# Optimization experiments

Hardware: AMD Instinct MI355X
Metric: run time of the kernel (lower is better)

The kernel has to match this reference:

```python
import jax, jax.numpy as jnp
import numpy as np

B, S, D_MODEL, D_K, D_V = 8, 2048, 1024, 1024, 1024


def setup_inputs() -> dict:
    key = jax.random.key(0)
    k1, k2, k3, k4 = jax.random.split(key, 4)
    x = jax.random.normal(k1, (B, S, D_MODEL), dtype=jnp.float32)
    # Store projection weights as [d_model, d_out] so projection is x @ W
    # (equivalent to torch Linear(d_model, d_out, bias=False) with W^T).
    scale = 1.0 / np.sqrt(D_MODEL)
    Wq = jax.random.normal(k2, (D_MODEL, D_K), dtype=jnp.float32) * scale
    Wk = jax.random.normal(k3, (D_MODEL, D_K), dtype=jnp.float32) * scale
    Wv = jax.random.normal(k4, (D_MODEL, D_V), dtype=jnp.float32) * scale
    return {"x": x, "Wq": Wq, "Wk": Wk, "Wv": Wv}


def reference(x, Wq, Wk, Wv):
    # Single-head causal self-attention, faithful to the original:
    # NOTE: the original scales by sqrt(x.shape[-1]) == sqrt(d_model),
    # not sqrt(d_k of the projection).
    Q = jnp.einsum('bsd,dk->bsk', x, Wq)
    K = jnp.einsum('bsd,dk->bsk', x, Wk)
    V = jnp.einsum('bsd,dv->bsv', x, Wv)
    inv_scale = 1.0 / jnp.sqrt(jnp.asarray(x.shape[-1], x.dtype))
    A = jnp.einsum('bqk,bsk->bqs', Q, K) * inv_scale  # [B, S, S]
    S_len = A.shape[-1]
    causal = jnp.tril(jnp.ones((S_len, S_len), dtype=bool))  # [S, S]
    A = jnp.where(causal, A, -jnp.inf)
    P = jax.nn.softmax(A, axis=-1)
    return jnp.einsum('bqs,bsv->bqv', P, V)
```

## Files before the change

### kernel.cpp

```cpp
#include <hip/hip_runtime.h>
#include <hip/hip_bf16.h>
#include <stdint.h>


typedef __bf16 bf16_t;
typedef __bf16 bf16x4 __attribute__((ext_vector_type(4)));
typedef __bf16 bf16x8 __attribute__((ext_vector_type(8)));
typedef float  floatx4 __attribute__((ext_vector_type(4)));

#define NB 8
#define SS 2048
#define DD 1024
#define INV_SCALE 0.03125f

__device__ __forceinline__ void async_ld16(const void* g, void* l) {
  __builtin_amdgcn_global_load_lds(
      (const __attribute__((address_space(1))) void*)g,
      (__attribute__((address_space(3))) void*)l, 16, 0, 0);
}

#define BARRIER() do { asm volatile("" ::: "memory"); \
  __builtin_amdgcn_s_barrier(); asm volatile("" ::: "memory"); } while (0)

__device__ __forceinline__ void mm256_core(
    const bf16_t* __restrict__ Ab, const bf16_t* __restrict__ Bb,
    int lda, int ldb, int nt,
    bf16_t* sA0, bf16_t* sA1, bf16_t* sA2, bf16_t* sA3,
    bf16_t* sB0, bf16_t* sB1, bf16_t* sB2, bf16_t* sB3,
    floatx4 acc[8][4]) {
  const int t    = threadIdx.x;
  const int lane = t & 63;
  const int wid  = t >> 6;
  const int wm   = wid >> 2;
  const int wn   = wid & 3;
  const int fm   = lane & 15;
  const int q    = lane >> 4;
  const int co   = (q ^ ((fm >> 1) & 3)) * 8;

  size_t goA[2], goB[2]; int lo[2];
#pragma unroll
  for (int k = 0; k < 2; ++k) {
    const int u   = k * 512 + t;
    const int row = u >> 2;
    const int cg  = (u & 3) ^ ((row >> 1) & 3);
    goA[k] = (size_t)row * lda + cg * 8;
    goB[k] = (size_t)row * ldb + cg * 8;
    lo[k]  = u * 8;
  }

  auto stage = [&](bf16_t* la, bf16_t* lb, int tile) {
    const size_t ko = (size_t)tile * 32;
    async_ld16(Ab + ko + goA[0], la + lo[0]);
    async_ld16(Ab + ko + goA[1], la + lo[1]);
    async_ld16(Bb + ko + goB[0], lb + lo[0]);
    async_ld16(Bb + ko + goB[1], lb + lo[1]);
  };

  const int paOff = (wm * 128 + fm) * 32;
  const int pbOff = (wn * 64 + fm) * 32;

  auto body = [&] __attribute__((always_inline)) (
      const bf16_t* AP, const bf16_t* BP, bf16_t* AN, bf16_t* BN, int T) {
    if (T + 3 < nt) {
      stage(AN, BN, T + 3);
      asm volatile("s_waitcnt vmcnt(12)" ::: "memory");
    } else if (T + 2 < nt) {
      asm volatile("s_waitcnt vmcnt(8)" ::: "memory");
    } else if (T + 1 < nt) {
      asm volatile("s_waitcnt vmcnt(4)" ::: "memory");
    } else {
      asm volatile("s_waitcnt vmcnt(0)" ::: "memory");
    }
    __builtin_amdgcn_s_barrier();
    asm volatile("" ::: "memory");

    const bf16_t* pa = AP + paOff;
    const bf16_t* pb = BP + pbOff;
    bf16x8 a0[4], a1[4], bv[4];
#pragma unroll
    for (int i = 0; i < 4; ++i) a0[i] = *(const bf16x8*)(pa + i * 512 + co);
#pragma unroll
    for (int j = 0; j < 4; ++j) bv[j] = *(const bf16x8*)(pb + j * 512 + co);
    __builtin_amdgcn_sched_barrier(0);
#pragma unroll
    for (int i = 0; i < 4; ++i) a1[i] = *(const bf16x8*)(pa + (4 + i) * 512 + co);

    asm volatile("s_waitcnt lgkmcnt(4)" ::: "memory");
    __builtin_amdgcn_sched_barrier(0);
    __builtin_amdgcn_s_setprio(1);
#pragma unroll
    for (int i = 0; i < 4; ++i)
#pragma unroll
      for (int j = 0; j < 4; ++j)
        acc[i][j] = __builtin_amdgcn_mfma_f32_16x16x32_bf16(bv[j], a0[i], acc[i][j], 0, 0, 0);
    __builtin_amdgcn_s_setprio(0);

    asm volatile("s_waitcnt lgkmcnt(0)" ::: "memory");
    __builtin_amdgcn_sched_barrier(0);
    __builtin_amdgcn_s_setprio(1);
#pragma unroll
    for (int i = 0; i < 4; ++i)
#pragma unroll
      for (int j = 0; j < 4; ++j)
        acc[4 + i][j] = __builtin_amdgcn_mfma_f32_16x16x32_bf16(bv[j], a1[i], acc[4 + i][j], 0, 0, 0);
    __builtin_amdgcn_s_setprio(0);
    asm volatile("" ::: "memory");
    __builtin_amdgcn_s_barrier();
  };

  stage(sA0, sB0, 0);
  stage(sA1, sB1, 1);
  stage(sA2, sB2, 2);

  for (int tb = 0; tb < nt; tb += 4) {
    body(sA0, sB0, sA3, sB3, tb + 0);
    body(sA1, sB1, sA0, sB0, tb + 1);
    body(sA2, sB2, sA1, sB1, tb + 2);
    body(sA3, sB3, sA2, sB2, tb + 3);
  }
}

__device__ __forceinline__ void zero_acc8(floatx4 acc[8][4]) {
#pragma unroll
  for (int i = 0; i < 8; ++i)
#pragma unroll
    for (int j = 0; j < 4; ++j)
      acc[i][j] = floatx4{0.f, 0.f, 0.f, 0.f};
}

__device__ __forceinline__ void store_c256_bf16(bf16_t* __restrict__ Cb, int ldc,
                                                floatx4 acc[8][4]) {
  const int lane = threadIdx.x & 63;
  const int wid  = threadIdx.x >> 6;
  const int wm = wid >> 2, wn = wid & 3;
  const int m0 = wm * 128 + (lane & 15);
  const int n0 = wn * 64 + (lane >> 4) * 4;
#pragma unroll
  for (int i = 0; i < 8; ++i)
#pragma unroll
    for (int j = 0; j < 4; ++j) {
      floatx4 a = acc[i][j];
      bf16x4 o = {(bf16_t)a[0], (bf16_t)a[1], (bf16_t)a[2], (bf16_t)a[3]};
      *(bf16x4*)(Cb + (size_t)(m0 + i * 16) * ldc + n0 + j * 16) = o;
    }
}

#define MM256_LDS_DECL                                                      \
  __shared__ __attribute__((aligned(16))) bf16_t sA0[8192], sA1[8192],      \
      sA2[8192], sA3[8192];                                                 \
  __shared__ __attribute__((aligned(16))) bf16_t sB0[8192], sB1[8192],      \
      sB2[8192], sB3[8192];

__device__ __forceinline__ void mm_core2(
    const bf16_t* __restrict__ Ab, const bf16_t* __restrict__ Bb,
    int lda, int ldb, int nt,
    bf16_t* sA0, bf16_t* sB0, bf16_t* sA1, bf16_t* sB1,
    floatx4 acc[4][4]) {
  const int t    = threadIdx.x;
  const int lane = t & 63;
  const int wm   = (t >> 6) >> 1;
  const int wn   = (t >> 6) & 1;
  const int fm   = lane & 15;
  const int q    = lane >> 4;
  const int xo   = fm & 7;

  size_t goA[4], goB[4]; int lo[4];
#pragma unroll
  for (int k = 0; k < 4; ++k) {
    const int u   = k * 256 + t;
    const int row = u >> 3;
    const int cc  = (u & 7) ^ (row & 7);
    goA[k] = (size_t)row * lda + cc * 8;
    goB[k] = (size_t)row * ldb + cc * 8;
    lo[k]  = u * 8;
  }

  auto stage = [&](bf16_t* la, bf16_t* lb, int tile) {
    const size_t ko = (size_t)tile * 64;
#pragma unroll
    for (int k = 0; k < 4; ++k) async_ld16(Ab + ko + goA[k], la + lo[k]);
#pragma unroll
    for (int k = 0; k < 4; ++k) async_ld16(Bb + ko + goB[k], lb + lo[k]);
  };

  const int paOff = (wm * 64 + fm) * 64;
  const int pbOff = (wn * 64 + fm) * 64;

  auto body = [&] __attribute__((always_inline)) (
      const bf16_t* CA, const bf16_t* CB, bf16_t* SA, bf16_t* SB, int T) {
    if (T + 1 < nt) {
      stage(SA, SB, T + 1);
      asm volatile("s_waitcnt vmcnt(8)" ::: "memory");
    } else {
      asm volatile("s_waitcnt vmcnt(0)" ::: "memory");
    }
    BARRIER();

    const bf16_t* pa = CA + paOff;
    const bf16_t* pb = CB + pbOff;
#pragma unroll
    for (int h = 0; h < 2; ++h) {
      const int co = ((h * 4 + q) ^ xo) * 8;
      bf16x8 af[4], bfr[4];
#pragma unroll
      for (int i = 0; i < 4; ++i) af[i]  = *(const bf16x8*)(pa + i * 1024 + co);
#pragma unroll
      for (int j = 0; j < 4; ++j) bfr[j] = *(const bf16x8*)(pb + j * 1024 + co);
      asm volatile("s_waitcnt lgkmcnt(0)" ::: "memory");
      __builtin_amdgcn_sched_barrier(0);
      __builtin_amdgcn_s_setprio(1);
#pragma unroll
      for (int i = 0; i < 4; ++i)
#pragma unroll
        for (int j = 0; j < 4; ++j)
          acc[i][j] = __builtin_amdgcn_mfma_f32_16x16x32_bf16(bfr[j], af[i], acc[i][j], 0, 0, 0);
      __builtin_amdgcn_s_setprio(0);
    }
    BARRIER();
  };

  stage(sA0, sB0, 0);
  for (int T = 0; T < nt; T += 2) {
    body(sA0, sB0, sA1, sB1, T);
    body(sA1, sB1, sA0, sB0, T + 1);
  }
}

__device__ __forceinline__ void zero_acc(floatx4 acc[4][4]) {
#pragma unroll
  for (int i = 0; i < 4; ++i)
#pragma unroll
    for (int j = 0; j < 4; ++j)
      acc[i][j] = floatx4{0.f, 0.f, 0.f, 0.f};
}

#define MM128_LDS_DECL                                                      \
  __shared__ __attribute__((aligned(16))) bf16_t sA0[128 * 64], sA1[128 * 64]; \
  __shared__ __attribute__((aligned(16))) bf16_t sB0[128 * 64], sB1[128 * 64];


__global__ __launch_bounds__(256) void prep(const float* __restrict__ x,
                                            const float* __restrict__ Wq,
                                            const float* __restrict__ Wk,
                                            const float* __restrict__ Wv,
                                            bf16_t* __restrict__ xb,
                                            bf16_t* __restrict__ Wt) {
  __shared__ float tile[32][33];
  const int bid = blockIdx.x;
  const int t = threadIdx.x;
  if (bid < 16384) {
    size_t i = (size_t)bid * 256 + t;
    float4 v = ((const float4*)x)[i];
    bf16x4 o = {(bf16_t)v.x, (bf16_t)v.y, (bf16_t)v.z, (bf16_t)v.w};
    ((bf16x4*)xb)[i] = o;
  } else {
    const int wb = bid - 16384;
    const int z = wb >> 10;
    const int rem = wb & 1023;
    const float* W = (z == 0) ? Wq : (z == 1 ? Wk : Wv);
    bf16_t* O = Wt + (size_t)z * DD * DD;
    const int ty = t >> 3;
    const int tx = t & 7;
    const int k0 = (rem >> 5) * 32, n0 = (rem & 31) * 32;
    float4 v = *(const float4*)(W + (size_t)(k0 + ty) * DD + n0 + tx * 4);
    tile[ty][tx * 4 + 0] = v.x;
    tile[ty][tx * 4 + 1] = v.y;
    tile[ty][tx * 4 + 2] = v.z;
    tile[ty][tx * 4 + 3] = v.w;
    __syncthreads();
    bf16x4 o = {(bf16_t)tile[tx * 4 + 0][ty], (bf16_t)tile[tx * 4 + 1][ty],
                (bf16_t)tile[tx * 4 + 2][ty], (bf16_t)tile[tx * 4 + 3][ty]};
    *(bf16x4*)(O + (size_t)(n0 + ty) * DD + k0 + tx * 4) = o;
  }
}


__global__ __launch_bounds__(512, 2) void qkproj_gemm(
    const bf16_t* __restrict__ xb, const bf16_t* __restrict__ Wt,
    bf16_t* __restrict__ QKb) {
  MM256_LDS_DECL
  const int mt = blockIdx.x, nt = blockIdx.y;
  const bf16_t* Ab = xb + (size_t)mt * 256 * DD;
  const bf16_t* Bb = Wt + (size_t)nt * 256 * DD;
  bf16_t* Cb = QKb + (size_t)mt * 256 * (2 * DD) + nt * 256;
  floatx4 acc[8][4];
  zero_acc8(acc);
  mm256_core(Ab, Bb, DD, DD, DD / 32,
             sA0, sA1, sA2, sA3, sB0, sB1, sB2, sB3, acc);
  store_c256_bf16(Cb, 2 * DD, acc);
}


__global__ __launch_bounds__(512, 2) void vproj_gemm(
    const bf16_t* __restrict__ xb, const bf16_t* __restrict__ Wt,
    bf16_t* __restrict__ VtB) {
  MM256_LDS_DECL
  const int bid = blockIdx.x;
  const int n = bid & 7;
  const int m = (bid >> 3) & 3;
  const int b = bid >> 5;
  const bf16_t* Ab = Wt + (size_t)2 * DD * DD + (size_t)m * 256 * DD;
  const bf16_t* Bb = xb + (size_t)b * SS * DD + (size_t)n * 256 * DD;
  bf16_t* Cb = VtB + (size_t)b * DD * SS + (size_t)m * 256 * SS + n * 256;
  floatx4 acc[8][4];
  zero_acc8(acc);
  mm256_core(Ab, Bb, DD, DD, DD / 32,
             sA0, sA1, sA2, sA3, sB0, sB1, sB2, sB3, acc);
  store_c256_bf16(Cb, SS, acc);
}


__global__ __launch_bounds__(256) void qk_p(
    const bf16_t* __restrict__ Q, const bf16_t* __restrict__ K,
    bf16_t* __restrict__ P, float* __restrict__ lpart) {
  const int b  = blockIdx.x & 7;
  const int tt = 135 - (blockIdx.x >> 3);
  int qi = (int)((sqrtf(8.0f * tt + 1.0f) - 1.0f) * 0.5f);
  while ((qi + 1) * (qi + 2) / 2 <= tt) ++qi;
  while (qi * (qi + 1) / 2 > tt) --qi;
  const int ki = tt - qi * (qi + 1) / 2;

  MM128_LDS_DECL
  __shared__ float reds[2][128];
  const bf16_t* Ab = Q + ((size_t)b * SS + qi * 128) * (size_t)(2 * DD);
  const bf16_t* Bb = K + ((size_t)b * SS + ki * 128) * (size_t)(2 * DD);
  floatx4 acc[4][4];
  zero_acc(acc);
  mm_core2(Ab, Bb, 2 * DD, 2 * DD, DD / 64, sA0, sB0, sA1, sB1, acc);

  const int lane = threadIdx.x & 63;
  const int wm = (threadIdx.x >> 6) >> 1, wn = (threadIdx.x >> 6) & 1;
  const bool diag = (ki == qi);
  bf16_t* Pb = P + (size_t)b * SS * SS;
  const int qloc0 = wm * 64 + (lane & 15);
  const int kvb0  = wn * 64 + (lane >> 4) * 4;

#pragma unroll
  for (int i = 0; i < 4; ++i) {
    const int qrow = qloc0 + i * 16;
    float partial = 0.f;
#pragma unroll
    for (int j = 0; j < 4; ++j) {
      const int kvb = kvb0 + j * 16;
      floatx4 p;
#pragma unroll
      for (int r = 0; r < 4; ++r) {
        const float s = acc[i][j][r] * INV_SCALE;
        p[r] = (diag && (kvb + r) > qrow) ? 0.f : __expf(s);
        partial += p[r];
      }
      bf16x4 o = {(bf16_t)p[0], (bf16_t)p[1], (bf16_t)p[2], (bf16_t)p[3]};
      *(bf16x4*)(Pb + (size_t)(qi * 128 + qrow) * SS + ki * 128 + kvb) = o;
    }
    partial += __shfl_xor(partial, 16);
    partial += __shfl_xor(partial, 32);
    if ((lane >> 4) == 0) reds[wn][qrow] = partial;
  }
  __syncthreads();
  const int t = threadIdx.x;
  if (t < 128) {
    size_t row = (size_t)b * SS + qi * 128 + t;
    lpart[row * 16 + ki] = reds[0][t] + reds[1][t];
  }
}


__global__ __launch_bounds__(256) void pv_gemm(
    const bf16_t* __restrict__ P, const bf16_t* __restrict__ Vt,
    const float* __restrict__ lpart, float* __restrict__ Out) {
  const int bid = blockIdx.x;
  const int b  = bid & 7;
  const int nj = (bid >> 3) & 7;
  const int qi = 15 - (bid >> 6);

  MM128_LDS_DECL
  __shared__ float sRl[128];
  const int t = threadIdx.x;
  if (t < 128) {
    const float* lp = lpart + ((size_t)b * SS + qi * 128 + t) * 16;
    float L = 0.f;
    for (int ci = 0; ci <= qi; ++ci) L += lp[ci];
    sRl[t] = 1.0f / L;
  }
  const bf16_t* Ab = P + (size_t)b * SS * SS + (size_t)qi * 128 * SS;
  const bf16_t* Bb = Vt + (size_t)b * DD * SS + (size_t)nj * 128 * SS;
  float* Cb = Out + (size_t)b * SS * DD + (size_t)qi * 128 * DD + nj * 128;
  floatx4 acc[4][4];
  zero_acc(acc);
  mm_core2(Ab, Bb, SS, SS, (qi + 1) * 2, sA0, sB0, sA1, sB1, acc);
  const int lane = threadIdx.x & 63;
  const int wm = (threadIdx.x >> 6) >> 1, wn = (threadIdx.x >> 6) & 1;
  const int m0 = wm * 64 + (lane & 15);
  const int n0 = wn * 64 + (lane >> 4) * 4;
#pragma unroll
  for (int i2 = 0; i2 < 4; ++i2) {
    const float scale = sRl[m0 + i2 * 16];
    float* crow = Cb + (size_t)(m0 + i2 * 16) * DD + n0;
#pragma unroll
    for (int j = 0; j < 4; ++j) {
      floatx4 o = acc[i2][j];
      o[0] *= scale; o[1] *= scale; o[2] *= scale; o[3] *= scale;
      *(floatx4*)(crow + j * 16) = o;
    }
  }
}


extern "C" void kernel_launch(void* const* d_in, const int* in_sizes, int n_in,
                              void* d_out, int out_size, void* d_ws, size_t ws_size,
                              hipStream_t stream) {
  const float* x  = (const float*)d_in[0];
  const float* Wq = (const float*)d_in[1];
  const float* Wk = (const float*)d_in[2];
  const float* Wv = (const float*)d_in[3];
  float* out = (float*)d_out;

  char* ws = (char*)d_ws;
  bf16_t* xb   = (bf16_t*)(ws);
  bf16_t* Wt   = (bf16_t*)(ws + 33554432ull);
  bf16_t* QKb  = (bf16_t*)(ws + 39845888ull);
  bf16_t* VtB  = (bf16_t*)(ws + 106954752ull);
  bf16_t* Pb   = (bf16_t*)(ws + 140509184ull);
  float*  lpart= (float*)(ws + 207618048ull);
  (void)in_sizes; (void)n_in; (void)out_size; (void)ws_size;

  prep<<<16384 + 3072, 256, 0, stream>>>(x, Wq, Wk, Wv, xb, Wt);
  qkproj_gemm<<<dim3(64, 8), 512, 0, stream>>>(xb, Wt, QKb);
  vproj_gemm<<<256, 512, 0, stream>>>(xb, Wt, VtB);
  qk_p<<<1088, 256, 0, stream>>>(QKb, QKb + DD, Pb, lpart);
  pv_gemm<<<1024, 256, 0, stream>>>(Pb, VtB, lpart, out);
}
```

Baseline: 351.1 us.

## Merge projection GEMMs and restructure both GEMM cores into 4-buffer prefetch-2 pipelines

Fuses the QK and V projection kernels into one 768-block launch. This removes a kernel boundary and the tail underutilisation between them. The 256 GEMM core changes from prefetch-depth-3 with two barriers per tile to prefetch-depth-2 with a single barrier per tile, using a 4-buffer ring. The 128 GEMM core used by qk_p and pv_gemm moves from a double-buffered K=64 tile to a quad-buffered K=32 tile with two tiles in flight, aiming at better latency hiding. This trades fewer barriers for a shallower or finer-grained pipeline and more loop iterations.

```diff
diff --git a/kernel.cpp b/kernel.cpp
--- a/kernel.cpp
+++ b/kernel.cpp
@@ -60,22 +60,19 @@
   const int pbOff = (wn * 64 + fm) * 32;
 
   auto body = [&] __attribute__((always_inline)) (
-      const bf16_t* AP, const bf16_t* BP, bf16_t* AN, bf16_t* BN, int T) {
-    if (T + 3 < nt) {
-      stage(AN, BN, T + 3);
-      asm volatile("s_waitcnt vmcnt(12)" ::: "memory");
-    } else if (T + 2 < nt) {
+      const bf16_t* CA, const bf16_t* CB, bf16_t* SA, bf16_t* SB, int T) {
+    if (T + 2 < nt) {
+      stage(SA, SB, T + 2);
       asm volatile("s_waitcnt vmcnt(8)" ::: "memory");
     } else if (T + 1 < nt) {
       asm volatile("s_waitcnt vmcnt(4)" ::: "memory");
     } else {
       asm volatile("s_waitcnt vmcnt(0)" ::: "memory");
     }
-    __builtin_amdgcn_s_barrier();
-    asm volatile("" ::: "memory");
-
-    const bf16_t* pa = AP + paOff;
-    const bf16_t* pb = BP + pbOff;
+    BARRIER();
+
+    const bf16_t* pa = CA + paOff;
+    const bf16_t* pb = CB + pbOff;
     bf16x8 a0[4], a1[4], bv[4];
 #pragma unroll
     for (int i = 0; i < 4; ++i) a0[i] = *(const bf16x8*)(pa + i * 512 + co);
@@ -104,19 +101,16 @@
       for (int j = 0; j < 4; ++j)
         acc[4 + i][j] = __builtin_amdgcn_mfma_f32_16x16x32_bf16(bv[j], a1[i], acc[4 + i][j], 0, 0, 0);
     __builtin_amdgcn_s_setprio(0);
-    asm volatile("" ::: "memory");
-    __builtin_amdgcn_s_barrier();
   };
 
   stage(sA0, sB0, 0);
   stage(sA1, sB1, 1);
-  stage(sA2, sB2, 2);
 
   for (int tb = 0; tb < nt; tb += 4) {
-    body(sA0, sB0, sA3, sB3, tb + 0);
-    body(sA1, sB1, sA0, sB0, tb + 1);
-    body(sA2, sB2, sA1, sB1, tb + 2);
-    body(sA3, sB3, sA2, sB2, tb + 3);
+    body(sA0, sB0, sA2, sB2, tb + 0);
+    body(sA1, sB1, sA3, sB3, tb + 1);
+    body(sA2, sB2, sA0, sB0, tb + 2);
+    body(sA3, sB3, sA1, sB1, tb + 3);
   }
 }
 
@@ -151,10 +145,11 @@
   __shared__ __attribute__((aligned(16))) bf16_t sB0[8192], sB1[8192],      \
       sB2[8192], sB3[8192];
 
-__device__ __forceinline__ void mm_core2(
+__device__ __forceinline__ void mm128_core(
     const bf16_t* __restrict__ Ab, const bf16_t* __restrict__ Bb,
     int lda, int ldb, int nt,
-    bf16_t* sA0, bf16_t* sB0, bf16_t* sA1, bf16_t* sB1,
+    bf16_t* sA0, bf16_t* sA1, bf16_t* sA2, bf16_t* sA3,
+    bf16_t* sB0, bf16_t* sB1, bf16_t* sB2, bf16_t* sB3,
     floatx4 acc[4][4]) {
   const int t    = threadIdx.x;
   const int lane = t & 63;
@@ -162,35 +157,37 @@
   const int wn   = (t >> 6) & 1;
   const int fm   = lane & 15;
   const int q    = lane >> 4;
-  const int xo   = fm & 7;
-
-  size_t goA[4], goB[4]; int lo[4];
-#pragma unroll
-  for (int k = 0; k < 4; ++k) {
+  const int co   = (q ^ ((fm >> 1) & 3)) * 8;
+
+  size_t goA[2], goB[2]; int lo[2];
+#pragma unroll
+  for (int k = 0; k < 2; ++k) {
     const int u   = k * 256 + t;
-    const int row = u >> 3;
-    const int cc  = (u & 7) ^ (row & 7);
-    goA[k] = (size_t)row * lda + cc * 8;
-    goB[k] = (size_t)row * ldb + cc * 8;
+    const int row = u >> 2;
+    const int cg  = (u & 3) ^ ((row >> 1) & 3);
+    goA[k] = (size_t)row * lda + cg * 8;
+    goB[k] = (size_t)row * ldb + cg * 8;
     lo[k]  = u * 8;
   }
 
   auto stage = [&](bf16_t* la, bf16_t* lb, int tile) {
-    const size_t ko = (size_t)tile * 64;
-#pragma unroll
-    for (int k = 0; k < 4; ++k) async_ld16(Ab + ko + goA[k], la + lo[k]);
-#pragma unroll
-    for (int k = 0; k < 4; ++k) async_ld16(Bb + ko + goB[k], lb + lo[k]);
+    const size_t ko = (size_t)tile * 32;
+    async_ld16(Ab + ko + goA[0], la + lo[0]);
+    async_ld16(Ab + ko + goA[1], la + lo[1]);
+    async_ld16(Bb + ko + goB[0], lb + lo[0]);
+    async_ld16(Bb + ko + goB[1], lb + lo[1]);
   };
 
-  const int paOff = (wm * 64 + fm) * 64;
-  const int pbOff = (wn * 64 + fm) * 64;
+  const int paOff = (wm * 64 + fm) * 32;
+  const int pbOff = (wn * 64 + fm) * 32;
 
   auto body = [&] __attribute__((always_inline)) (
       const bf16_t* CA, const bf16_t* CB, bf16_t* SA, bf16_t* SB, int T) {
-    if (T + 1 < nt) {
-      stage(SA, SB, T + 1);
+    if (T + 2 < nt) {
+      stage(SA, SB, T + 2);
       asm volatile("s_waitcnt vmcnt(8)" ::: "memory");
+    } else if (T + 1 < nt) {
+      asm volatile("s_waitcnt vmcnt(4)" ::: "memory");
     } else {
       asm volatile("s_waitcnt vmcnt(0)" ::: "memory");
     }
@@ -198,31 +195,29 @@
 
     const bf16_t* pa = CA + paOff;
     const bf16_t* pb = CB + pbOff;
-#pragma unroll
-    for (int h = 0; h < 2; ++h) {
-      const int co = ((h * 4 + q) ^ xo) * 8;
-      bf16x8 af[4], bfr[4];
-#pragma unroll
-      for (int i = 0; i < 4; ++i) af[i]  = *(const bf16x8*)(pa + i * 1024 + co);
-#pragma unroll
-      for (int j = 0; j < 4; ++j) bfr[j] = *(const bf16x8*)(pb + j * 1024 + co);
-      asm volatile("s_waitcnt lgkmcnt(0)" ::: "memory");
-      __builtin_amdgcn_sched_barrier(0);
-      __builtin_amdgcn_s_setprio(1);
-#pragma unroll
-      for (int i = 0; i < 4; ++i)
-#pragma unroll
-        for (int j = 0; j < 4; ++j)
-          acc[i][j] = __builtin_amdgcn_mfma_f32_16x16x32_bf16(bfr[j], af[i], acc[i][j], 0, 0, 0);
-      __builtin_amdgcn_s_setprio(0);
-    }
-    BARRIER();
+    bf16x8 af[4], bv[4];
+#pragma unroll
+    for (int i = 0; i < 4; ++i) af[i] = *(const bf16x8*)(pa + i * 512 + co);
+#pragma unroll
+    for (int j = 0; j < 4; ++j) bv[j] = *(const bf16x8*)(pb + j * 512 + co);
+    asm volatile("s_waitcnt lgkmcnt(0)" ::: "memory");
+    __builtin_amdgcn_sched_barrier(0);
+    __builtin_amdgcn_s_setprio(1);
+#pragma unroll
+    for (int i = 0; i < 4; ++i)
+#pragma unroll
+      for (int j = 0; j < 4; ++j)
+        acc[i][j] = __builtin_amdgcn_mfma_f32_16x16x32_bf16(bv[j], af[i], acc[i][j], 0, 0, 0);
+    __builtin_amdgcn_s_setprio(0);
   };
 
   stage(sA0, sB0, 0);
-  for (int T = 0; T < nt; T += 2) {
-    body(sA0, sB0, sA1, sB1, T);
-    body(sA1, sB1, sA0, sB0, T + 1);
+  stage(sA1, sB1, 1);
+  for (int tb = 0; tb < nt; tb += 4) {
+    body(sA0, sB0, sA2, sB2, tb + 0);
+    body(sA1, sB1, sA3, sB3, tb + 1);
+    body(sA2, sB2, sA0, sB0, tb + 2);
+    body(sA3, sB3, sA1, sB1, tb + 3);
   }
 }
 
@@ -235,8 +230,10 @@
 }
 
 #define MM128_LDS_DECL                                                      \
-  __shared__ __attribute__((aligned(16))) bf16_t sA0[128 * 64], sA1[128 * 64]; \
-  __shared__ __attribute__((aligned(16))) bf16_t sB0[128 * 64], sB1[128 * 64];
+  __shared__ __attribute__((aligned(16))) bf16_t sA0[4096], sA1[4096],      \
+      sA2[4096], sA3[4096];                                                 \
+  __shared__ __attribute__((aligned(16))) bf16_t sB0[4096], sB1[4096],      \
+      sB2[4096], sB3[4096];
 
 
 __global__ __launch_bounds__(256) void prep(const float* __restrict__ x,
@@ -275,38 +272,33 @@
 }
 
 
-__global__ __launch_bounds__(512, 2) void qkproj_gemm(
+__global__ __launch_bounds__(512, 2) void proj_gemm(
     const bf16_t* __restrict__ xb, const bf16_t* __restrict__ Wt,
-    bf16_t* __restrict__ QKb) {
+    bf16_t* __restrict__ QKb, bf16_t* __restrict__ VtB) {
   MM256_LDS_DECL
-  const int mt = blockIdx.x, nt = blockIdx.y;
-  const bf16_t* Ab = xb + (size_t)mt * 256 * DD;
-  const bf16_t* Bb = Wt + (size_t)nt * 256 * DD;
-  bf16_t* Cb = QKb + (size_t)mt * 256 * (2 * DD) + nt * 256;
+  const int bid = blockIdx.x;
+  const bf16_t* Ab;
+  const bf16_t* Bb;
+  bf16_t* Cb;
+  if (bid < 512) {
+    const int mt = bid & 63, nt2 = bid >> 6;
+    Ab = xb + (size_t)mt * 256 * DD;
+    Bb = Wt + (size_t)nt2 * 256 * DD;
+    Cb = QKb + (size_t)mt * 256 * (2 * DD) + nt2 * 256;
+  } else {
+    const int r = bid - 512;
+    const int n = r & 7;
+    const int m = (r >> 3) & 3;
+    const int b = r >> 5;
+    Ab = Wt + (size_t)2 * DD * DD + (size_t)m * 256 * DD;
+    Bb = xb + (size_t)b * SS * DD + (size_t)n * 256 * DD;
+    Cb = VtB + (size_t)b * DD * SS + (size_t)m * 256 * SS + n * 256;
+  }
   floatx4 acc[8][4];
   zero_acc8(acc);
   mm256_core(Ab, Bb, DD, DD, DD / 32,
              sA0, sA1, sA2, sA3, sB0, sB1, sB2, sB3, acc);
-  store_c256_bf16(Cb, 2 * DD, acc);
-}
-
-
-__global__ __launch_bounds__(512, 2) void vproj_gemm(
-    const bf16_t* __restrict__ xb, const bf16_t* __restrict__ Wt,
-    bf16_t* __restrict__ VtB) {
-  MM256_LDS_DECL
-  const int bid = blockIdx.x;
-  const int n = bid & 7;
-  const int m = (bid >> 3) & 3;
-  const int b = bid >> 5;
-  const bf16_t* Ab = Wt + (size_t)2 * DD * DD + (size_t)m * 256 * DD;
-  const bf16_t* Bb = xb + (size_t)b * SS * DD + (size_t)n * 256 * DD;
-  bf16_t* Cb = VtB + (size_t)b * DD * SS + (size_t)m * 256 * SS + n * 256;
-  floatx4 acc[8][4];
-  zero_acc8(acc);
-  mm256_core(Ab, Bb, DD, DD, DD / 32,
-             sA0, sA1, sA2, sA3, sB0, sB1, sB2, sB3, acc);
-  store_c256_bf16(Cb, SS, acc);
+  store_c256_bf16(Cb, 2048, acc);
 }
 
 
@@ -326,7 +318,8 @@
   const bf16_t* Bb = K + ((size_t)b * SS + ki * 128) * (size_t)(2 * DD);
   floatx4 acc[4][4];
   zero_acc(acc);
-  mm_core2(Ab, Bb, 2 * DD, 2 * DD, DD / 64, sA0, sB0, sA1, sB1, acc);
+  mm128_core(Ab, Bb, 2 * DD, 2 * DD, DD / 32,
+             sA0, sA1, sA2, sA3, sB0, sB1, sB2, sB3, acc);
 
   const int lane = threadIdx.x & 63;
   const int wm = (threadIdx.x >> 6) >> 1, wn = (threadIdx.x >> 6) & 1;
@@ -387,7 +380,8 @@
   float* Cb = Out + (size_t)b * SS * DD + (size_t)qi * 128 * DD + nj * 128;
   floatx4 acc[4][4];
   zero_acc(acc);
-  mm_core2(Ab, Bb, SS, SS, (qi + 1) * 2, sA0, sB0, sA1, sB1, acc);
+  mm128_core(Ab, Bb, SS, SS, (qi + 1) * 4,
+             sA0, sA1, sA2, sA3, sB0, sB1, sB2, sB3, acc);
   const int lane = threadIdx.x & 63;
   const int wm = (threadIdx.x >> 6) >> 1, wn = (threadIdx.x >> 6) & 1;
   const int m0 = wm * 64 + (lane & 15);
@@ -425,8 +419,7 @@
   (void)in_sizes; (void)n_in; (void)out_size; (void)ws_size;
 
   prep<<<16384 + 3072, 256, 0, stream>>>(x, Wq, Wk, Wv, xb, Wt);
-  qkproj_gemm<<<dim3(64, 8), 512, 0, stream>>>(xb, Wt, QKb);
-  vproj_gemm<<<256, 512, 0, stream>>>(xb, Wt, VtB);
+  proj_gemm<<<768, 512, 0, stream>>>(xb, Wt, QKb, VtB);
   qk_p<<<1088, 256, 0, stream>>>(QKb, QKb + DD, Pb, lpart);
   pv_gemm<<<1024, 256, 0, stream>>>(Pb, VtB, lpart, out);
 }
```

After: 351.1 us. Within noise of the previous version (-0.0%).
